# Kernel optimization log

Measured on AMD Instinct MI355X. Metric: run time of the kernel, lower is better.

## Reference

```python
import jax, jax.numpy as jnp
import numpy as np

Q_INTERVAL = 4          # opt.interval
Q = 2 ** Q_INTERVAL     # 16, quantization bin width
L = 2 ** (8 - Q_INTERVAL) + 1  # 17, LUT side length
OUT_C = 3
BD = 1                  # padding for mode 's'


def setup_inputs() -> dict:
    key = jax.random.key(0)
    k_img, k_w = jax.random.split(key)
    # 8-bit pixel values stored as float32 (the torch module does // and % on floats)
    img_in = jax.random.randint(k_img, (8, 1, 513, 513), 0, 256).astype(jnp.float32)
    # LUT parameter, stored as float in [-1, 1] (npy / 127.0 in the original)
    weight = jax.random.uniform(k_w, (L ** 4, OUT_C), dtype=jnp.float32,
                                minval=-1.0, maxval=1.0)
    return {"img_in": img_in, "weight": weight}


def _interp_s(img_in, weight):
    """Mode 's' quadrilinear (4-simplex) LUT interpolation, faithful to
    SWF2LUT.InterpTorchBatch. The 24 explicit permutation cases in the torch
    code are exactly the descending sort of the four fractional parts
    (ties broken toward the later pixel: d before c before b before a)."""
    # weight quantization: round to int levels in [-127, 127]
    w = jnp.clip(jnp.round(weight * 127.0), -127.0, 127.0)

    h = img_in.shape[2] - BD
    ww = img_in.shape[3] - BD
    # 2x2 neighborhood (mode 's')
    a = img_in[:, :, 0:h,     0:ww]
    b = img_in[:, :, 0:h,     1:1 + ww]
    c = img_in[:, :, 1:1 + h, 0:ww]
    d = img_in[:, :, 1:1 + h, 1:1 + ww]

    ia = jnp.floor_divide(a, Q).astype(jnp.int32)
    ib = jnp.floor_divide(b, Q).astype(jnp.int32)
    ic = jnp.floor_divide(c, Q).astype(jnp.int32)
    idd = jnp.floor_divide(d, Q).astype(jnp.int32)

    f = jnp.stack([a % Q, b % Q, c % Q, d % Q], axis=-1)  # (B,C,h,w,4)

    # Descending sort with ties broken so that larger index (d,c,b,a) comes
    # first -- matches the strict '>' case ordering of the torch code.
    tie_key = f * 4.0 + jnp.arange(4, dtype=f.dtype)
    order = jnp.argsort(-tie_key, axis=-1)                 # (B,C,h,w,4)
    fs = jnp.take_along_axis(f, order, axis=-1)            # sorted desc

    strides = jnp.array([L ** 3, L ** 2, L, 1], dtype=jnp.int32)
    base = ia * (L ** 3) + ib * (L ** 2) + ic * L + idd    # (B,C,h,w)
    sstrides = strides[order]                              # (B,C,h,w,4)
    cum = jnp.cumsum(sstrides, axis=-1)
    # 5 simplex vertices: base, then incrementally add strides in sort order
    idx = jnp.concatenate([base[..., None], base[..., None] + cum], axis=-1)

    p = w[idx]                                             # (B,C,h,w,5,outC)
    wts = jnp.stack([Q - fs[..., 0],
                     fs[..., 0] - fs[..., 1],
                     fs[..., 1] - fs[..., 2],
                     fs[..., 2] - fs[..., 3],
                     fs[..., 3]], axis=-1)                 # (B,C,h,w,5)
    out = jnp.sum(wts[..., None] * p, axis=-2) / Q         # (B,C,h,w,outC)
    return out


def reference(img_in, weight):
    return _interp_s(img_in, weight)
```

## Files before the change

kernel.cpp:

```cpp
#include <hip/hip_runtime.h>
#include <stdint.h>


#define LQ   17
#define L2C  (17 * 17)
#define L3C  (17 * 17 * 17)
#define NENT (L3C * 17)
#define PLANE_STRIDE 83584
#define LDS_BYTES   83584
#define SUMSTRIDE (L3C + L2C + LQ + 1)

__device__ __forceinline__ int stride_of(int j) {
    return j == 0 ? L3C : (j == 1 ? L2C : (j == 2 ? LQ : 1));
}

__global__ __launch_bounds__(256) void quant_planar_kernel(
    const float* __restrict__ w, char* __restrict__ planes, int n) {
    int e = blockIdx.x * 256 + threadIdx.x;
    if (e >= n) return;
#pragma unroll
    for (int ch = 0; ch < 3; ++ch) {
        int q = (int)rintf(w[e * 3 + ch] * 127.0f);
        q = min(127, max(-127, q));
        planes[ch * PLANE_STRIDE + e] = (char)q;
    }
}

extern __shared__ char lut[];

__global__ __launch_bounds__(1024) void interp_fused_kernel(
    const float* __restrict__ img, const char* __restrict__ planes,
    float* __restrict__ out) {
    int G = blockIdx.x * 1024 + threadIdx.x;
    int x0 = (G & 63) << 3;
    int y  = (G >> 6) & 511;
    int im = G >> 15;

    const float* r0 = img + im * (513 * 513) + y * 513 + x0;
    const float* r1 = r0 + 513;
    float v0[9], v1[9];
#pragma unroll
    for (int i = 0; i < 9; ++i) { v0[i] = r0[i]; v1[i] = r1[i]; }

    int pi0[8], pk1[8], pk2[8];
#pragma unroll
    for (int i = 0; i < 8; ++i) {
        int a = (int)v0[i], b = (int)v0[i + 1];
        int c = (int)v1[i], d = (int)v1[i + 1];
        int base = (a >> 4) * L3C + (b >> 4) * L2C + (c >> 4) * LQ + (d >> 4);
        int k0 = ((a & 15) << 2) | 0;
        int k1 = ((b & 15) << 2) | 1;
        int k2 = ((c & 15) << 2) | 2;
        int k3 = ((d & 15) << 2) | 3;
        int t;
        if (k0 < k1) { t = k0; k0 = k1; k1 = t; }
        if (k2 < k3) { t = k2; k2 = k3; k3 = t; }
        if (k0 < k2) { t = k0; k0 = k2; k2 = t; }
        if (k1 < k3) { t = k1; k1 = k3; k3 = t; }
        if (k1 < k2) { t = k1; k1 = k2; k2 = t; }
        int fs0 = k0 >> 2, fs1 = k1 >> 2, fs2 = k2 >> 2, fs3 = k3 >> 2;
        int s0 = stride_of(k0 & 3);
        int s01 = s0 + stride_of(k1 & 3);
        int s012 = s01 + stride_of(k2 & 3);
        pi0[i] = base;
        pk1[i] = s0 | (s01 << 13);
        pk2[i] = (fs0 << 12) | (fs1 << 8) | (fs2 << 4) | fs3 | (s012 << 16);
    }

    int racc[3][4];
#pragma unroll
    for (int ch = 0; ch < 3; ++ch)
#pragma unroll
        for (int p = 0; p < 4; ++p) racc[ch][p] = 0;

#pragma unroll
    for (int ch = 0; ch < 3; ++ch) {
        __syncthreads();
        {
            const uint4* src =
                (const uint4*)(planes + (size_t)ch * PLANE_STRIDE);
            uint4* dst = (uint4*)lut;
            for (int k = threadIdx.x; k < PLANE_STRIDE / 16; k += 1024)
                dst[k] = src[k];
        }
        __syncthreads();
        const signed char* t8 = (const signed char*)lut;
#pragma unroll
        for (int i = 0; i < 8; ++i) {
            int fs = pk2[i];
            int fs0 = (fs >> 12) & 15, fs1 = (fs >> 8) & 15;
            int fs2 = (fs >> 4) & 15,  fs3 = fs & 15;
            int i0 = pi0[i];
            int i1 = i0 + (pk1[i] & 0x1FFF);
            int i2 = i0 + (pk1[i] >> 13);
            int i3 = i0 + ((fs >> 16) & 0x1FFF);
            int i4 = i0 + SUMSTRIDE;
            int p0 = t8[i0];
            int p1 = t8[i1];
            int p2 = t8[i2];
            int p3 = t8[i3];
            int p4 = t8[i4];
            int acc = (16 - fs0) * p0 + (fs0 - fs1) * p1 + (fs1 - fs2) * p2 +
                      (fs2 - fs3) * p3 + fs3 * p4;
            racc[ch][i >> 1] |= (acc & 0xFFFF) << (16 * (i & 1));
        }
    }

    float res[24];
#pragma unroll
    for (int ch = 0; ch < 3; ++ch)
#pragma unroll
        for (int p = 0; p < 4; ++p) {
            int lo = (racc[ch][p] << 16) >> 16;
            int hi = racc[ch][p] >> 16;
            res[(2 * p) * 3 + ch]     = (float)lo * 0.0625f;
            res[(2 * p + 1) * 3 + ch] = (float)hi * 0.0625f;
        }

    int opix = ((im * 512 + y) * 512 + x0) * 3;
    float4* o = (float4*)(out + opix);
#pragma unroll
    for (int q = 0; q < 6; ++q)
        o[q] = make_float4(res[q * 4], res[q * 4 + 1], res[q * 4 + 2],
                           res[q * 4 + 3]);
}

__global__ __launch_bounds__(256) void quant_pack_kernel(
    const float* __restrict__ w, uint32_t* __restrict__ tab, int n) {
    int e = blockIdx.x * 256 + threadIdx.x;
    if (e >= n) return;
    int q0 = (int)rintf(w[e * 3 + 0] * 127.0f);
    int q1 = (int)rintf(w[e * 3 + 1] * 127.0f);
    int q2 = (int)rintf(w[e * 3 + 2] * 127.0f);
    q0 = min(127, max(-127, q0));
    q1 = min(127, max(-127, q1));
    q2 = min(127, max(-127, q2));
    tab[e] = (uint32_t)(q0 & 0xFF) | ((uint32_t)(q1 & 0xFF) << 8) |
             ((uint32_t)(q2 & 0xFF) << 16);
}

__global__ __launch_bounds__(256) void interp_packed_kernel(
    const float* __restrict__ img, const uint32_t* __restrict__ tab,
    float* __restrict__ out) {
    int gid = blockIdx.x * 256 + threadIdx.x;
    int x0 = (gid & 127) << 2;
    int y  = (gid >> 7) & 511;
    int im = gid >> 16;

    const float* r0 = img + im * (513 * 513) + y * 513 + x0;
    const float* r1 = r0 + 513;
    float v0[5], v1[5];
#pragma unroll
    for (int i = 0; i < 5; ++i) { v0[i] = r0[i]; v1[i] = r1[i]; }

    float res[12];
#pragma unroll
    for (int i = 0; i < 4; ++i) {
        int a = (int)v0[i], b = (int)v0[i + 1];
        int c = (int)v1[i], d = (int)v1[i + 1];
        int base = (a >> 4) * L3C + (b >> 4) * L2C + (c >> 4) * LQ + (d >> 4);
        int k0 = ((a & 15) << 2) | 0;
        int k1 = ((b & 15) << 2) | 1;
        int k2 = ((c & 15) << 2) | 2;
        int k3 = ((d & 15) << 2) | 3;
        int t;
        if (k0 < k1) { t = k0; k0 = k1; k1 = t; }
        if (k2 < k3) { t = k2; k2 = k3; k3 = t; }
        if (k0 < k2) { t = k0; k0 = k2; k2 = t; }
        if (k1 < k3) { t = k1; k1 = k3; k3 = t; }
        if (k1 < k2) { t = k1; k1 = k2; k2 = t; }
        int fs0 = k0 >> 2, fs1 = k1 >> 2, fs2 = k2 >> 2, fs3 = k3 >> 2;
        int s0 = stride_of(k0 & 3);
        int s1 = stride_of(k1 & 3);
        int s2 = stride_of(k2 & 3);
        int i0 = base;
        int i1 = base + s0;
        int i2 = i1 + s1;
        int i3 = i2 + s2;
        int i4 = base + SUMSTRIDE;
        uint32_t u0 = tab[i0], u1 = tab[i1], u2 = tab[i2], u3 = tab[i3],
                 u4 = tab[i4];
        int w0 = 16 - fs0, w1 = fs0 - fs1, w2 = fs1 - fs2, w3 = fs2 - fs3,
            w4 = fs3;
#pragma unroll
        for (int chn = 0; chn < 3; ++chn) {
            int sh = 24 - chn * 8;
            int p0 = (int)(u0 << sh) >> 24;
            int p1 = (int)(u1 << sh) >> 24;
            int p2 = (int)(u2 << sh) >> 24;
            int p3 = (int)(u3 << sh) >> 24;
            int p4 = (int)(u4 << sh) >> 24;
            int acc = w0 * p0 + w1 * p1 + w2 * p2 + w3 * p3 + w4 * p4;
            res[i * 3 + chn] = (float)acc * 0.0625f;
        }
    }

    int opix = ((im * 512 + y) * 512 + x0) * 3;
    float4* o = (float4*)(out + opix);
    o[0] = make_float4(res[0], res[1], res[2], res[3]);
    o[1] = make_float4(res[4], res[5], res[6], res[7]);
    o[2] = make_float4(res[8], res[9], res[10], res[11]);
}

extern "C" void kernel_launch(void* const* d_in, const int* in_sizes, int n_in,
                              void* d_out, int out_size, void* d_ws,
                              size_t ws_size, hipStream_t stream) {
    const float* img = (const float*)d_in[0];
    const float* wgt = (const float*)d_in[1];
    float* out = (float*)d_out;

    const size_t planes_bytes = (size_t)3 * PLANE_STRIDE;

    bool lds_ok = (ws_size >= planes_bytes) && (d_ws != nullptr);
    if (lds_ok) {
        hipError_t e = hipFuncSetAttribute(
            reinterpret_cast<const void*>(interp_fused_kernel),
            hipFuncAttributeMaxDynamicSharedMemorySize, LDS_BYTES);
        lds_ok = (e == hipSuccess);
    }

    if (lds_ok) {
        char* planes = (char*)d_ws;
        quant_planar_kernel<<<(NENT + 255) / 256, 256, 0, stream>>>(
            wgt, planes, NENT);
        interp_fused_kernel<<<256, 1024, LDS_BYTES, stream>>>(img, planes,
                                                              out);
    } else if (ws_size >= (size_t)NENT * sizeof(uint32_t) && d_ws != nullptr) {
        uint32_t* tab = (uint32_t*)d_ws;
        quant_pack_kernel<<<(NENT + 255) / 256, 256, 0, stream>>>(wgt, tab,
                                                                  NENT);
        interp_packed_kernel<<<8 * 512 * 128 / 256, 256, 0, stream>>>(
            img, tab, out);
    }
}
```

Baseline: 36.43 us.

## Pack two LUT channels as 16-bit in LDS and prefetch third channel plane

Replaces three per-channel LDS plane loads with two phases. The first phase stages a 16-bit table holding channels 0 and 1 for the first 81920 entries (160 KB of LDS), with a global-memory fallback for the few bases whose vertices fall outside that range. The second phase stages the channel-2 byte plane, which is prefetched into registers while phase one runs. This cuts the number of barrier-separated LUT reload passes from three to two and overlaps the channel-2 fetch with compute, at the cost of more LDS, more registers and a divergent fallback path. Image rows are also loaded with packed float4 reads.

```diff
diff --git a/kernel.cpp b/kernel.cpp
--- a/kernel.cpp
+++ b/kernel.cpp
@@ -6,41 +6,60 @@
 #define L2C  (17 * 17)
 #define L3C  (17 * 17 * 17)
 #define NENT (L3C * 17)
-#define PLANE_STRIDE 83584
-#define LDS_BYTES   83584
 #define SUMSTRIDE (L3C + L2C + LQ + 1)
+
+#define LDSA_ENTRIES 81920
+#define LDSA_BYTES   163840
+#define RARE_BASE    (LDSA_ENTRIES - SUMSTRIDE)
+#define P16_ENTRIES  83968
+#define CH2_BYTES    98304
+
+__global__ __launch_bounds__(256) void quant_split_kernel(
+    const float* __restrict__ w, uint16_t* __restrict__ p16,
+    char* __restrict__ ch2) {
+    int e = blockIdx.x * 256 + threadIdx.x;
+    if (e < NENT) {
+        int q0 = (int)rintf(w[e * 3 + 0] * 127.0f);
+        int q1 = (int)rintf(w[e * 3 + 1] * 127.0f);
+        int q2 = (int)rintf(w[e * 3 + 2] * 127.0f);
+        q0 = min(127, max(-127, q0));
+        q1 = min(127, max(-127, q1));
+        q2 = min(127, max(-127, q2));
+        p16[e] = (uint16_t)((q0 & 0xFF) | ((q1 & 0xFF) << 8));
+        ch2[e] = (char)q2;
+    } else {
+        if (e < P16_ENTRIES) p16[e] = 0;
+        ch2[e] = 0;
+    }
+}
 
 __device__ __forceinline__ int stride_of(int j) {
     return j == 0 ? L3C : (j == 1 ? L2C : (j == 2 ? LQ : 1));
 }
 
-__global__ __launch_bounds__(256) void quant_planar_kernel(
-    const float* __restrict__ w, char* __restrict__ planes, int n) {
-    int e = blockIdx.x * 256 + threadIdx.x;
-    if (e >= n) return;
-#pragma unroll
-    for (int ch = 0; ch < 3; ++ch) {
-        int q = (int)rintf(w[e * 3 + ch] * 127.0f);
-        q = min(127, max(-127, q));
-        planes[ch * PLANE_STRIDE + e] = (char)q;
-    }
+struct __attribute__((packed, aligned(4))) f4p { float a, b, c, d; };
+__device__ __forceinline__ void load9(const float* p, float v[9]) {
+    const f4p* q = (const f4p*)p;
+    f4p A = q[0], B = q[1];
+    v[0] = A.a; v[1] = A.b; v[2] = A.c; v[3] = A.d;
+    v[4] = B.a; v[5] = B.b; v[6] = B.c; v[7] = B.d;
+    v[8] = p[8];
 }
 
 extern __shared__ char lut[];
 
-__global__ __launch_bounds__(1024) void interp_fused_kernel(
-    const float* __restrict__ img, const char* __restrict__ planes,
-    float* __restrict__ out) {
+__global__ __launch_bounds__(1024) void interp_fused16_kernel(
+    const float* __restrict__ img, const uint16_t* __restrict__ p16,
+    const char* __restrict__ ch2, float* __restrict__ out) {
     int G = blockIdx.x * 1024 + threadIdx.x;
     int x0 = (G & 63) << 3;
     int y  = (G >> 6) & 511;
     int im = G >> 15;
 
     const float* r0 = img + im * (513 * 513) + y * 513 + x0;
-    const float* r1 = r0 + 513;
     float v0[9], v1[9];
-#pragma unroll
-    for (int i = 0; i < 9; ++i) { v0[i] = r0[i]; v1[i] = r1[i]; }
+    load9(r0, v0);
+    load9(r0 + 513, v1);
 
     int pi0[8], pk1[8], pk2[8];
 #pragma unroll
@@ -67,55 +86,95 @@
         pk2[i] = (fs0 << 12) | (fs1 << 8) | (fs2 << 4) | fs3 | (s012 << 16);
     }
 
-    int racc[3][4];
-#pragma unroll
-    for (int ch = 0; ch < 3; ++ch)
-#pragma unroll
-        for (int p = 0; p < 4; ++p) racc[ch][p] = 0;
-
-#pragma unroll
-    for (int ch = 0; ch < 3; ++ch) {
-        __syncthreads();
-        {
-            const uint4* src =
-                (const uint4*)(planes + (size_t)ch * PLANE_STRIDE);
-            uint4* dst = (uint4*)lut;
-            for (int k = threadIdx.x; k < PLANE_STRIDE / 16; k += 1024)
-                dst[k] = src[k];
+    {
+        const uint4* src = (const uint4*)p16;
+        uint4* dst = (uint4*)lut;
+        for (int k = threadIdx.x; k < LDSA_BYTES / 16; k += 1024)
+            dst[k] = src[k];
+    }
+    __syncthreads();
+
+    const uint4* c2src = (const uint4*)ch2;
+    uint4 pf0 = c2src[threadIdx.x];
+    uint4 pf1 = c2src[threadIdx.x + 1024];
+    uint4 pf2 = c2src[threadIdx.x + 2048];
+    uint4 pf3 = c2src[threadIdx.x + 3072];
+    uint4 pf4 = c2src[threadIdx.x + 4096];
+    uint4 pf5 = c2src[threadIdx.x + 5120];
+
+    const uint16_t* t16 = (const uint16_t*)lut;
+    int racc0[4] = {0, 0, 0, 0};
+    int racc1[4] = {0, 0, 0, 0};
+#pragma unroll
+    for (int i = 0; i < 8; ++i) {
+        int fs = pk2[i];
+        int fs0 = (fs >> 12) & 15, fs1 = (fs >> 8) & 15;
+        int fs2 = (fs >> 4) & 15,  fs3 = fs & 15;
+        int i0 = pi0[i];
+        int i1 = i0 + (pk1[i] & 0x1FFF);
+        int i2 = i0 + (pk1[i] >> 13);
+        int i3 = i0 + ((fs >> 16) & 0x1FFF);
+        int i4 = i0 + SUMSTRIDE;
+        int u0, u1, u2, u3, u4;
+        if (__builtin_expect(i0 < RARE_BASE, 1)) {
+            u0 = t16[i0]; u1 = t16[i1]; u2 = t16[i2];
+            u3 = t16[i3]; u4 = t16[i4];
+        } else {
+            u0 = p16[i0]; u1 = p16[i1]; u2 = p16[i2];
+            u3 = p16[i3]; u4 = p16[i4];
         }
-        __syncthreads();
-        const signed char* t8 = (const signed char*)lut;
-#pragma unroll
-        for (int i = 0; i < 8; ++i) {
-            int fs = pk2[i];
-            int fs0 = (fs >> 12) & 15, fs1 = (fs >> 8) & 15;
-            int fs2 = (fs >> 4) & 15,  fs3 = fs & 15;
-            int i0 = pi0[i];
-            int i1 = i0 + (pk1[i] & 0x1FFF);
-            int i2 = i0 + (pk1[i] >> 13);
-            int i3 = i0 + ((fs >> 16) & 0x1FFF);
-            int i4 = i0 + SUMSTRIDE;
-            int p0 = t8[i0];
-            int p1 = t8[i1];
-            int p2 = t8[i2];
-            int p3 = t8[i3];
-            int p4 = t8[i4];
-            int acc = (16 - fs0) * p0 + (fs0 - fs1) * p1 + (fs1 - fs2) * p2 +
-                      (fs2 - fs3) * p3 + fs3 * p4;
-            racc[ch][i >> 1] |= (acc & 0xFFFF) << (16 * (i & 1));
-        }
+        int w0 = 16 - fs0, w1 = fs0 - fs1, w2 = fs1 - fs2, w3 = fs2 - fs3,
+            w4 = fs3;
+        int a0 = w0 * ((int)(u0 << 24) >> 24) + w1 * ((int)(u1 << 24) >> 24) +
+                 w2 * ((int)(u2 << 24) >> 24) + w3 * ((int)(u3 << 24) >> 24) +
+                 w4 * ((int)(u4 << 24) >> 24);
+        int a1 = w0 * ((int)(u0 << 16) >> 24) + w1 * ((int)(u1 << 16) >> 24) +
+                 w2 * ((int)(u2 << 16) >> 24) + w3 * ((int)(u3 << 16) >> 24) +
+                 w4 * ((int)(u4 << 16) >> 24);
+        racc0[i >> 1] |= (a0 & 0xFFFF) << (16 * (i & 1));
+        racc1[i >> 1] |= (a1 & 0xFFFF) << (16 * (i & 1));
+    }
+    __syncthreads();
+
+    {
+        uint4* dst = (uint4*)lut;
+        dst[threadIdx.x]        = pf0;
+        dst[threadIdx.x + 1024] = pf1;
+        dst[threadIdx.x + 2048] = pf2;
+        dst[threadIdx.x + 3072] = pf3;
+        dst[threadIdx.x + 4096] = pf4;
+        dst[threadIdx.x + 5120] = pf5;
+    }
+    __syncthreads();
+
+    const signed char* t8 = (const signed char*)lut;
+    int racc2[4] = {0, 0, 0, 0};
+#pragma unroll
+    for (int i = 0; i < 8; ++i) {
+        int fs = pk2[i];
+        int fs0 = (fs >> 12) & 15, fs1 = (fs >> 8) & 15;
+        int fs2 = (fs >> 4) & 15,  fs3 = fs & 15;
+        int i0 = pi0[i];
+        int p0 = t8[i0];
+        int p1 = t8[i0 + (pk1[i] & 0x1FFF)];
+        int p2 = t8[i0 + (pk1[i] >> 13)];
+        int p3 = t8[i0 + ((fs >> 16) & 0x1FFF)];
+        int p4 = t8[i0 + SUMSTRIDE];
+        int acc = (16 - fs0) * p0 + (fs0 - fs1) * p1 + (fs1 - fs2) * p2 +
+                  (fs2 - fs3) * p3 + fs3 * p4;
+        racc2[i >> 1] |= (acc & 0xFFFF) << (16 * (i & 1));
     }
 
     float res[24];
 #pragma unroll
-    for (int ch = 0; ch < 3; ++ch)
-#pragma unroll
-        for (int p = 0; p < 4; ++p) {
-            int lo = (racc[ch][p] << 16) >> 16;
-            int hi = racc[ch][p] >> 16;
-            res[(2 * p) * 3 + ch]     = (float)lo * 0.0625f;
-            res[(2 * p + 1) * 3 + ch] = (float)hi * 0.0625f;
-        }
+    for (int p = 0; p < 4; ++p) {
+        res[(2 * p) * 3 + 0]     = (float)((racc0[p] << 16) >> 16) * 0.0625f;
+        res[(2 * p + 1) * 3 + 0] = (float)(racc0[p] >> 16) * 0.0625f;
+        res[(2 * p) * 3 + 1]     = (float)((racc1[p] << 16) >> 16) * 0.0625f;
+        res[(2 * p + 1) * 3 + 1] = (float)(racc1[p] >> 16) * 0.0625f;
+        res[(2 * p) * 3 + 2]     = (float)((racc2[p] << 16) >> 16) * 0.0625f;
+        res[(2 * p + 1) * 3 + 2] = (float)(racc2[p] >> 16) * 0.0625f;
+    }
 
     int opix = ((im * 512 + y) * 512 + x0) * 3;
     float4* o = (float4*)(out + opix);
@@ -125,37 +184,37 @@
                            res[q * 4 + 3]);
 }
 
-__global__ __launch_bounds__(256) void quant_pack_kernel(
-    const float* __restrict__ w, uint32_t* __restrict__ tab, int n) {
+#define PLANE_STRIDE 83584
+#define LDS8_BYTES   83584
+
+__global__ __launch_bounds__(256) void quant_planar_kernel(
+    const float* __restrict__ w, char* __restrict__ planes, int n) {
     int e = blockIdx.x * 256 + threadIdx.x;
     if (e >= n) return;
-    int q0 = (int)rintf(w[e * 3 + 0] * 127.0f);
-    int q1 = (int)rintf(w[e * 3 + 1] * 127.0f);
-    int q2 = (int)rintf(w[e * 3 + 2] * 127.0f);
-    q0 = min(127, max(-127, q0));
-    q1 = min(127, max(-127, q1));
-    q2 = min(127, max(-127, q2));
-    tab[e] = (uint32_t)(q0 & 0xFF) | ((uint32_t)(q1 & 0xFF) << 8) |
-             ((uint32_t)(q2 & 0xFF) << 16);
-}
-
-__global__ __launch_bounds__(256) void interp_packed_kernel(
-    const float* __restrict__ img, const uint32_t* __restrict__ tab,
+#pragma unroll
+    for (int ch = 0; ch < 3; ++ch) {
+        int q = (int)rintf(w[e * 3 + ch] * 127.0f);
+        q = min(127, max(-127, q));
+        planes[ch * PLANE_STRIDE + e] = (char)q;
+    }
+}
+
+__global__ __launch_bounds__(1024) void interp_fused8_kernel(
+    const float* __restrict__ img, const char* __restrict__ planes,
     float* __restrict__ out) {
-    int gid = blockIdx.x * 256 + threadIdx.x;
-    int x0 = (gid & 127) << 2;
-    int y  = (gid >> 7) & 511;
-    int im = gid >> 16;
+    int G = blockIdx.x * 1024 + threadIdx.x;
+    int x0 = (G & 63) << 3;
+    int y  = (G >> 6) & 511;
+    int im = G >> 15;
 
     const float* r0 = img + im * (513 * 513) + y * 513 + x0;
-    const float* r1 = r0 + 513;
-    float v0[5], v1[5];
-#pragma unroll
-    for (int i = 0; i < 5; ++i) { v0[i] = r0[i]; v1[i] = r1[i]; }
-
-    float res[12];
-#pragma unroll
-    for (int i = 0; i < 4; ++i) {
+    float v0[9], v1[9];
+    load9(r0, v0);
+    load9(r0 + 513, v1);
+
+    int pi0[8], pk1[8], pk2[8];
+#pragma unroll
+    for (int i = 0; i < 8; ++i) {
         int a = (int)v0[i], b = (int)v0[i + 1];
         int c = (int)v1[i], d = (int)v1[i + 1];
         int base = (a >> 4) * L3C + (b >> 4) * L2C + (c >> 4) * LQ + (d >> 4);
@@ -171,35 +230,64 @@
         if (k1 < k2) { t = k1; k1 = k2; k2 = t; }
         int fs0 = k0 >> 2, fs1 = k1 >> 2, fs2 = k2 >> 2, fs3 = k3 >> 2;
         int s0 = stride_of(k0 & 3);
-        int s1 = stride_of(k1 & 3);
-        int s2 = stride_of(k2 & 3);
-        int i0 = base;
-        int i1 = base + s0;
-        int i2 = i1 + s1;
-        int i3 = i2 + s2;
-        int i4 = base + SUMSTRIDE;
-        uint32_t u0 = tab[i0], u1 = tab[i1], u2 = tab[i2], u3 = tab[i3],
-                 u4 = tab[i4];
-        int w0 = 16 - fs0, w1 = fs0 - fs1, w2 = fs1 - fs2, w3 = fs2 - fs3,
-            w4 = fs3;
-#pragma unroll
-        for (int chn = 0; chn < 3; ++chn) {
-            int sh = 24 - chn * 8;
-            int p0 = (int)(u0 << sh) >> 24;
-            int p1 = (int)(u1 << sh) >> 24;
-            int p2 = (int)(u2 << sh) >> 24;
-            int p3 = (int)(u3 << sh) >> 24;
-            int p4 = (int)(u4 << sh) >> 24;
-            int acc = w0 * p0 + w1 * p1 + w2 * p2 + w3 * p3 + w4 * p4;
-            res[i * 3 + chn] = (float)acc * 0.0625f;
+        int s01 = s0 + stride_of(k1 & 3);
+        int s012 = s01 + stride_of(k2 & 3);
+        pi0[i] = base;
+        pk1[i] = s0 | (s01 << 13);
+        pk2[i] = (fs0 << 12) | (fs1 << 8) | (fs2 << 4) | fs3 | (s012 << 16);
+    }
+
+    int racc[3][4];
+#pragma unroll
+    for (int ch = 0; ch < 3; ++ch)
+#pragma unroll
+        for (int p = 0; p < 4; ++p) racc[ch][p] = 0;
+
+#pragma unroll
+    for (int ch = 0; ch < 3; ++ch) {
+        __syncthreads();
+        {
+            const uint4* src =
+                (const uint4*)(planes + (size_t)ch * PLANE_STRIDE);
+            uint4* dst = (uint4*)lut;
+            for (int k = threadIdx.x; k < PLANE_STRIDE / 16; k += 1024)
+                dst[k] = src[k];
         }
-    }
+        __syncthreads();
+        const signed char* t8 = (const signed char*)lut;
+#pragma unroll
+        for (int i = 0; i < 8; ++i) {
+            int fs = pk2[i];
+            int fs0 = (fs >> 12) & 15, fs1 = (fs >> 8) & 15;
+            int fs2 = (fs >> 4) & 15,  fs3 = fs & 15;
+            int i0 = pi0[i];
+            int p0 = t8[i0];
+            int p1 = t8[i0 + (pk1[i] & 0x1FFF)];
+            int p2 = t8[i0 + (pk1[i] >> 13)];
+            int p3 = t8[i0 + ((fs >> 16) & 0x1FFF)];
+            int p4 = t8[i0 + SUMSTRIDE];
+            int acc = (16 - fs0) * p0 + (fs0 - fs1) * p1 + (fs1 - fs2) * p2 +
+                      (fs2 - fs3) * p3 + fs3 * p4;
+            racc[ch][i >> 1] |= (acc & 0xFFFF) << (16 * (i & 1));
+        }
+    }
+
+    float res[24];
+#pragma unroll
+    for (int ch = 0; ch < 3; ++ch)
+#pragma unroll
+        for (int p = 0; p < 4; ++p) {
+            res[(2 * p) * 3 + ch] =
+                (float)((racc[ch][p] << 16) >> 16) * 0.0625f;
+            res[(2 * p + 1) * 3 + ch] = (float)(racc[ch][p] >> 16) * 0.0625f;
+        }
 
     int opix = ((im * 512 + y) * 512 + x0) * 3;
     float4* o = (float4*)(out + opix);
-    o[0] = make_float4(res[0], res[1], res[2], res[3]);
-    o[1] = make_float4(res[4], res[5], res[6], res[7]);
-    o[2] = make_float4(res[8], res[9], res[10], res[11]);
+#pragma unroll
+    for (int q = 0; q < 6; ++q)
+        o[q] = make_float4(res[q * 4], res[q * 4 + 1], res[q * 4 + 2],
+                           res[q * 4 + 3]);
 }
 
 extern "C" void kernel_launch(void* const* d_in, const int* in_sizes, int n_in,
@@ -209,27 +297,38 @@
     const float* wgt = (const float*)d_in[1];
     float* out = (float*)d_out;
 
+    const size_t p16_bytes = (size_t)P16_ENTRIES * 2;
+    const size_t need16 = p16_bytes + CH2_BYTES;
+    bool ok16 = (ws_size >= need16) && (d_ws != nullptr);
+    if (ok16) {
+        hipError_t e = hipFuncSetAttribute(
+            reinterpret_cast<const void*>(interp_fused16_kernel),
+            hipFuncAttributeMaxDynamicSharedMemorySize, LDSA_BYTES);
+        ok16 = (e == hipSuccess);
+    }
+    if (ok16) {
+        uint16_t* p16 = (uint16_t*)d_ws;
+        char* ch2 = (char*)d_ws + p16_bytes;
+        quant_split_kernel<<<CH2_BYTES / 256, 256, 0, stream>>>(wgt, p16,
+                                                                ch2);
+        interp_fused16_kernel<<<256, 1024, LDSA_BYTES, stream>>>(img, p16,
+                                                                 ch2, out);
+        return;
+    }
+
     const size_t planes_bytes = (size_t)3 * PLANE_STRIDE;
-
-    bool lds_ok = (ws_size >= planes_bytes) && (d_ws != nullptr);
-    if (lds_ok) {
+    bool ok8 = (ws_size >= planes_bytes) && (d_ws != nullptr);
+    if (ok8) {
         hipError_t e = hipFuncSetAttribute(
-            reinterpret_cast<const void*>(interp_fused_kernel),
-            hipFuncAttributeMaxDynamicSharedMemorySize, LDS_BYTES);
-        lds_ok = (e == hipSuccess);
-    }
-
-    if (lds_ok) {
+            reinterpret_cast<const void*>(interp_fused8_kernel),
+            hipFuncAttributeMaxDynamicSharedMemorySize, LDS8_BYTES);
+        ok8 = (e == hipSuccess);
+    }
+    if (ok8) {
         char* planes = (char*)d_ws;
         quant_planar_kernel<<<(NENT + 255) / 256, 256, 0, stream>>>(
             wgt, planes, NENT);
-        interp_fused_kernel<<<256, 1024, LDS_BYTES, stream>>>(img, planes,
-                                                              out);
-    } else if (ws_size >= (size_t)NENT * sizeof(uint32_t) && d_ws != nullptr) {
-        uint32_t* tab = (uint32_t*)d_ws;
-        quant_pack_kernel<<<(NENT + 255) / 256, 256, 0, stream>>>(wgt, tab,
-                                                                  NENT);
-        interp_packed_kernel<<<8 * 512 * 128 / 256, 256, 0, stream>>>(
-            img, tab, out);
-    }
-}
+        interp_fused8_kernel<<<256, 1024, LDS8_BYTES, stream>>>(img, planes,
+                                                                out);
+    }
+}
```

Result: slower. 40.86 us (+12.2%).
